# Kernel optimization log

Measured on AMD Instinct MI355X. Metric: run time of the kernel, lower is better.

The kernel has to match this reference:

```python
import jax, jax.numpy as jnp
import numpy as np

N = 50000
E = 800000
IN_C = 128
HID = 64
HEADS = 4
OUT_C = 64
NEG_SLOPE = 0.2


def _glorot(key, shape):
    fan = shape[0] + shape[-1]
    return jax.random.normal(key, shape, dtype=jnp.float32) * jnp.sqrt(2.0 / fan)


def setup_inputs() -> dict:
    key = jax.random.key(0)
    ks = jax.random.split(key, 12)
    x = jax.random.normal(ks[0], (N, IN_C), dtype=jnp.float32)
    edge_index = jax.random.randint(ks[1], (2, E), 0, N, dtype=jnp.int64)
    edge_attr = jax.random.normal(ks[2], (E, 8), dtype=jnp.float32)
    # gat1: in -> heads*hid
    W1 = _glorot(ks[3], (IN_C, HEADS * HID))
    att_src1 = _glorot(ks[4], (HEADS, HID))
    att_dst1 = _glorot(ks[5], (HEADS, HID))
    b1 = jnp.zeros((HEADS * HID,), dtype=jnp.float32)
    # gat2: heads*hid -> out, 1 head
    W2 = _glorot(ks[6], (HEADS * HID, OUT_C))
    att_src2 = _glorot(ks[7], (1, OUT_C))
    att_dst2 = _glorot(ks[8], (1, OUT_C))
    b2 = jnp.zeros((OUT_C,), dtype=jnp.float32)
    return {"x": x, "edge_index": edge_index, "edge_attr": edge_attr,
            "W1": W1, "att_src1": att_src1, "att_dst1": att_dst1, "b1": b1,
            "W2": W2, "att_src2": att_src2, "att_dst2": att_dst2, "b2": b2}


def _gat_conv(x, src, dst, W, att_src, att_dst, b, heads, n_nodes):
    # x: [N, Cin] -> h: [N, H, C]
    h = (x @ W).reshape(n_nodes, heads, -1)
    a_src = jnp.sum(h * att_src, axis=-1)  # [N, H]
    a_dst = jnp.sum(h * att_dst, axis=-1)  # [N, H]
    e = jax.nn.leaky_relu(a_src[src] + a_dst[dst], NEG_SLOPE)  # [Etot, H]
    # segment softmax over destination node (self-loops guarantee non-empty segments)
    m = jax.ops.segment_max(e, dst, num_segments=n_nodes)      # [N, H]
    w = jnp.exp(e - m[dst])
    denom = jax.ops.segment_sum(w, dst, num_segments=n_nodes)  # [N, H]
    alpha = w / (denom[dst] + 1e-16)                           # [Etot, H]
    out = jax.ops.segment_sum(alpha[:, :, None] * h[src], dst, num_segments=n_nodes)
    return out.reshape(n_nodes, -1) + b  # concat heads (identity when heads==1)


def reference(x, edge_index, edge_attr, W1, att_src1, att_dst1, b1, W2, att_src2, att_dst2, b2):
    # PyG GATConv with edge_dim=None ignores edge_attr; add_self_loops=True by default.
    loop = jnp.arange(N, dtype=edge_index.dtype)
    src = jnp.concatenate([edge_index[0], loop])
    dst = jnp.concatenate([edge_index[1], loop])
    h = jax.nn.elu(_gat_conv(x, src, dst, W1, att_src1, att_dst1, b1, HEADS, N))
    out = jax.nn.elu(_gat_conv(h, src, dst, W2, att_src2, att_dst2, b2, 1, N))
    return out
```

## Files before the change

### kernel.cpp

```cpp
#include <hip/hip_runtime.h>
#include <hip/hip_bf16.h>
#include <math.h>

#define LEAKY 0.2f

#define BM 64
#define BN 64
#define BK 32
__global__ __launch_bounds__(256) void gemm_f32(const float* __restrict__ A,
                                                const float* __restrict__ B,
                                                float* __restrict__ C,
                                                int M, int K, int NC) {
    __shared__ float As[BK][BM + 1];
    __shared__ float Bs[BK][BN];
    const int tid = threadIdx.x;
    const int bm = blockIdx.x * BM;
    const int bn = blockIdx.y * BN;
    const int tx = tid & 15, ty = tid >> 4;
    float acc[4][4] = {};
    for (int k0 = 0; k0 < K; k0 += BK) {
        #pragma unroll
        for (int i = 0; i < (BM * BK) / 256; ++i) {
            int idx = tid + i * 256;
            int r = idx >> 5, c = idx & 31;
            int gr = bm + r;
            As[c][r] = (gr < M) ? A[gr * K + k0 + c] : 0.f;
        }
        #pragma unroll
        for (int i = 0; i < (BK * BN) / 256; ++i) {
            int idx = tid + i * 256;
            int r = idx >> 6, c = idx & 63;
            Bs[r][c] = B[(k0 + r) * NC + bn + c];
        }
        __syncthreads();
        #pragma unroll
        for (int k = 0; k < BK; ++k) {
            float a[4], b[4];
            #pragma unroll
            for (int i = 0; i < 4; ++i) a[i] = As[k][ty * 4 + i];
            #pragma unroll
            for (int j = 0; j < 4; ++j) b[j] = Bs[k][tx * 4 + j];
            #pragma unroll
            for (int i = 0; i < 4; ++i)
                #pragma unroll
                for (int j = 0; j < 4; ++j)
                    acc[i][j] += a[i] * b[j];
        }
        __syncthreads();
    }
    #pragma unroll
    for (int i = 0; i < 4; ++i) {
        int gr = bm + ty * 4 + i;
        if (gr < M) {
            #pragma unroll
            for (int j = 0; j < 4; ++j)
                C[gr * NC + bn + tx * 4 + j] = acc[i][j];
        }
    }
}

__global__ __launch_bounds__(256) void attn_scores(const float* __restrict__ h,
                                                   const float* __restrict__ att_s,
                                                   const float* __restrict__ att_d,
                                                   float* __restrict__ asrc,
                                                   float* __restrict__ adst,
                                                   int nN, int HC) {
    int idx = blockIdx.x * 256 + threadIdx.x;
    int lane = threadIdx.x & 63;
    int n = idx / HC;
    int w = idx - n * HC;
    if (n >= nN) return;
    float hv = h[(size_t)n * HC + w];
    float vs = hv * att_s[w];
    float vd = hv * att_d[w];
    #pragma unroll
    for (int off = 32; off > 0; off >>= 1) {
        vs += __shfl_down(vs, off);
        vd += __shfl_down(vd, off);
    }
    if (lane == 0) {
        int head = w >> 6;
        int H = HC >> 6;
        asrc[n * H + head] = vs;
        adst[n * H + head] = vd;
    }
}

__global__ __launch_bounds__(256) void count_deg(const int* __restrict__ ei, int E_, int N_,
                                                 int* __restrict__ deg) {
    int eid = blockIdx.x * 256 + threadIdx.x;
    int Etot = E_ + N_;
    if (eid >= Etot) return;
    int dst = (eid < E_) ? ei[E_ + eid] : (eid - E_);
    atomicAdd(&deg[dst], 1);
}

__global__ __launch_bounds__(1024) void scan_offsets(const int* __restrict__ deg,
                                                     int* __restrict__ off, int n) {
    __shared__ int wsum[16];
    int tid = threadIdx.x;
    int lane = tid & 63, w = tid >> 6;
    int chunk = (n + 1023) / 1024;
    int b = tid * chunk;
    int e = min(b + chunk, n);
    int s = 0;
    for (int i = b; i < e; ++i) s += deg[i];
    int v = s;
    #pragma unroll
    for (int o = 1; o < 64; o <<= 1) {
        int t = __shfl_up(v, o);
        if (lane >= o) v += t;
    }
    if (lane == 63) wsum[w] = v;
    __syncthreads();
    if (w == 0) {
        int t = (lane < 16) ? wsum[lane] : 0;
        #pragma unroll
        for (int o = 1; o < 16; o <<= 1) {
            int u = __shfl_up(t, o);
            if (lane >= o) t += u;
        }
        if (lane < 16) wsum[lane] = t;
    }
    __syncthreads();
    int acc = (w > 0 ? wsum[w - 1] : 0) + (v - s);
    for (int i = b; i < e; ++i) { off[i] = acc; acc += deg[i]; }
    if (e == n) off[n] = acc;
}

__global__ __launch_bounds__(256) void scatter_edges(const int* __restrict__ ei, int E_, int N_,
                                                     int* __restrict__ off,
                                                     int* __restrict__ csr) {
    int eid = blockIdx.x * 256 + threadIdx.x;
    int Etot = E_ + N_;
    if (eid >= Etot) return;
    int src, dst;
    if (eid < E_) { src = ei[eid]; dst = ei[E_ + eid]; }
    else          { src = dst = eid - E_; }
    int pos = atomicAdd(&off[dst], 1);
    csr[pos] = src;
}

__global__ __launch_bounds__(256) void gat_agg_h4(const int* __restrict__ off,
                                                  const int* __restrict__ csr,
                                                  const float* __restrict__ asrc,
                                                  const float* __restrict__ adst,
                                                  const float* __restrict__ hsrc,
                                                  const float* __restrict__ bias,
                                                  float* __restrict__ outp, int N_) {
    int wv = threadIdx.x >> 6, lane = threadIdx.x & 63;
    int node = blockIdx.x * 4 + wv;
    if (node >= N_) return;
    int s = node ? off[node - 1] : 0;
    int e = off[node];
    float4 ad = *(const float4*)(adst + node * 4);
    float m0 = -INFINITY, m1 = -INFINITY, m2 = -INFINITY, m3 = -INFINITY;
    for (int i = s + lane; i < e; i += 64) {
        int u = csr[i];
        float4 as = *(const float4*)(asrc + u * 4);
        float e0 = as.x + ad.x; e0 = e0 > 0.f ? e0 : LEAKY * e0; m0 = fmaxf(m0, e0);
        float e1 = as.y + ad.y; e1 = e1 > 0.f ? e1 : LEAKY * e1; m1 = fmaxf(m1, e1);
        float e2 = as.z + ad.z; e2 = e2 > 0.f ? e2 : LEAKY * e2; m2 = fmaxf(m2, e2);
        float e3 = as.w + ad.w; e3 = e3 > 0.f ? e3 : LEAKY * e3; m3 = fmaxf(m3, e3);
    }
    #pragma unroll
    for (int o = 32; o > 0; o >>= 1) {
        m0 = fmaxf(m0, __shfl_xor(m0, o));
        m1 = fmaxf(m1, __shfl_xor(m1, o));
        m2 = fmaxf(m2, __shfl_xor(m2, o));
        m3 = fmaxf(m3, __shfl_xor(m3, o));
    }
    float a0 = 0.f, a1 = 0.f, a2 = 0.f, a3 = 0.f;
    float d0 = 0.f, d1 = 0.f, d2 = 0.f, d3 = 0.f;
    for (int i = s; i < e; ++i) {
        int u = csr[i];
        float4 as = *(const float4*)(asrc + u * 4);
        float e0 = as.x + ad.x; e0 = e0 > 0.f ? e0 : LEAKY * e0; float w0 = __expf(e0 - m0);
        float e1 = as.y + ad.y; e1 = e1 > 0.f ? e1 : LEAKY * e1; float w1 = __expf(e1 - m1);
        float e2 = as.z + ad.z; e2 = e2 > 0.f ? e2 : LEAKY * e2; float w2 = __expf(e2 - m2);
        float e3 = as.w + ad.w; e3 = e3 > 0.f ? e3 : LEAKY * e3; float w3 = __expf(e3 - m3);
        d0 += w0; d1 += w1; d2 += w2; d3 += w3;
        const float* hp = hsrc + (size_t)u * 256 + lane;
        a0 += w0 * hp[0];
        a1 += w1 * hp[64];
        a2 += w2 * hp[128];
        a3 += w3 * hp[192];
    }
    size_t ob = (size_t)node * 256 + lane;
    float v;
    v = a0 / (d0 + 1e-16f) + bias[lane];       outp[ob]       = v > 0.f ? v : expm1f(v);
    v = a1 / (d1 + 1e-16f) + bias[lane + 64];  outp[ob + 64]  = v > 0.f ? v : expm1f(v);
    v = a2 / (d2 + 1e-16f) + bias[lane + 128]; outp[ob + 128] = v > 0.f ? v : expm1f(v);
    v = a3 / (d3 + 1e-16f) + bias[lane + 192]; outp[ob + 192] = v > 0.f ? v : expm1f(v);
}

__global__ __launch_bounds__(256) void gat_agg_h1(const int* __restrict__ off,
                                                  const int* __restrict__ csr,
                                                  const float* __restrict__ asrc,
                                                  const float* __restrict__ adst,
                                                  const float* __restrict__ g,
                                                  const float* __restrict__ bias,
                                                  float* __restrict__ outp, int N_) {
    int wv = threadIdx.x >> 6, lane = threadIdx.x & 63;
    int node = blockIdx.x * 4 + wv;
    if (node >= N_) return;
    int s = node ? off[node - 1] : 0;
    int e = off[node];
    float ad = adst[node];
    float mm = -INFINITY;
    for (int i = s + lane; i < e; i += 64) {
        float ev = asrc[csr[i]] + ad;
        ev = ev > 0.f ? ev : LEAKY * ev;
        mm = fmaxf(mm, ev);
    }
    #pragma unroll
    for (int o = 32; o > 0; o >>= 1) mm = fmaxf(mm, __shfl_xor(mm, o));
    float a = 0.f, d = 0.f;
    for (int i = s; i < e; ++i) {
        int u = csr[i];
        float ev = asrc[u] + ad;
        ev = ev > 0.f ? ev : LEAKY * ev;
        float w = __expf(ev - mm);
        d += w;
        a += w * g[(size_t)u * 64 + lane];
    }
    float v = a / (d + 1e-16f) + bias[lane];
    outp[(size_t)node * 64 + lane] = v > 0.f ? v : expm1f(v);
}

extern "C" void kernel_launch(void* const* d_in, const int* in_sizes, int n_in,
                              void* d_out, int out_size, void* d_ws, size_t ws_size,
                              hipStream_t stream) {
    const float* x        = (const float*)d_in[0];
    const int*   ei       = (const int*)d_in[1];
    const float* W1       = (const float*)d_in[3];
    const float* att_src1 = (const float*)d_in[4];
    const float* att_dst1 = (const float*)d_in[5];
    const float* b1       = (const float*)d_in[6];
    const float* W2       = (const float*)d_in[7];
    const float* att_src2 = (const float*)d_in[8];
    const float* att_dst2 = (const float*)d_in[9];
    const float* b2       = (const float*)d_in[10];
    float* out = (float*)d_out;

    const int N = in_sizes[0] / 128;
    const int E = in_sizes[1] / 2;
    const int Etot = E + N;

    float* ws    = (float*)d_ws;
    float* h1    = ws;
    float* h2    = h1 + (size_t)N * 256;
    float* g2    = h1;
    float* asrc1 = h2 + (size_t)N * 256;
    float* adst1 = asrc1 + (size_t)N * 4;
    float* asrc2 = adst1 + (size_t)N * 4;
    float* adst2 = asrc2 + N;
    int*   deg   = (int*)(adst2 + N);
    int*   off   = deg + (N + 1);
    int*   csr   = off + (N + 1);

    hipMemsetAsync(deg, 0, (N + 1) * sizeof(int), stream);
    count_deg<<<(Etot + 255) / 256, 256, 0, stream>>>(ei, E, N, deg);
    scan_offsets<<<1, 1024, 0, stream>>>(deg, off, N);
    scatter_edges<<<(Etot + 255) / 256, 256, 0, stream>>>(ei, E, N, off, csr);

    {
        dim3 g((N + BM - 1) / BM, 256 / BN);
        gemm_f32<<<g, 256, 0, stream>>>(x, W1, h1, N, 128, 256);
    }
    attn_scores<<<(N * 256) / 256, 256, 0, stream>>>(h1, att_src1, att_dst1, asrc1, adst1, N, 256);
    gat_agg_h4<<<(N + 3) / 4, 256, 0, stream>>>(off, csr, asrc1, adst1, h1, b1, h2, N);

    {
        dim3 g((N + BM - 1) / BM, 64 / BN);
        gemm_f32<<<g, 256, 0, stream>>>(h2, W2, g2, N, 256, 64);
    }
    attn_scores<<<(N * 64) / 256, 256, 0, stream>>>(g2, att_src2, att_dst2, asrc2, adst2, N, 64);
    gat_agg_h1<<<(N + 3) / 4, 256, 0, stream>>>(off, csr, asrc2, adst2, g2, b2, out, N);
}
```

Before: 628.4 us.

## Fuse attention-score dot products into GEMM epilogue and split h4 aggregation per head

The attention score reductions are computed inside the GEMM epilogue through a 16-lane shuffle reduction, which removes the two separate attn_scores launches and their re-reads of h. The 4-head aggregation kernel now uses one block per node with one wave per head, so each wave handles a single head instead of all four. This spreads the per-node serial edge loop across four waves, but each wave now repeats the CSR index and score loads.

Measured after the change: 705.6 us. +12.3%, slower.

```diff
diff --git a/kernel.cpp b/kernel.cpp
--- a/kernel.cpp
+++ b/kernel.cpp
@@ -7,9 +7,13 @@
 #define BM 64
 #define BN 64
 #define BK 32
-__global__ __launch_bounds__(256) void gemm_f32(const float* __restrict__ A,
+__global__ __launch_bounds__(256) void gemm_att(const float* __restrict__ A,
                                                 const float* __restrict__ B,
                                                 float* __restrict__ C,
+                                                const float* __restrict__ att_s,
+                                                const float* __restrict__ att_d,
+                                                float* __restrict__ asrc,
+                                                float* __restrict__ adst,
                                                 int M, int K, int NC) {
     __shared__ float As[BK][BM + 1];
     __shared__ float Bs[BK][BN];
@@ -24,13 +28,13 @@
             int idx = tid + i * 256;
             int r = idx >> 5, c = idx & 31;
             int gr = bm + r;
-            As[c][r] = (gr < M) ? A[gr * K + k0 + c] : 0.f;
+            As[c][r] = (gr < M) ? A[(size_t)gr * K + k0 + c] : 0.f;
         }
         #pragma unroll
         for (int i = 0; i < (BK * BN) / 256; ++i) {
             int idx = tid + i * 256;
             int r = idx >> 6, c = idx & 63;
-            Bs[r][c] = B[(k0 + r) * NC + bn + c];
+            Bs[r][c] = B[(size_t)(k0 + r) * NC + bn + c];
         }
         __syncthreads();
         #pragma unroll
@@ -48,41 +52,37 @@
         }
         __syncthreads();
     }
+    float s_att[4], d_att[4];
+    #pragma unroll
+    for (int j = 0; j < 4; ++j) {
+        s_att[j] = att_s[bn + tx * 4 + j];
+        d_att[j] = att_d[bn + tx * 4 + j];
+    }
+    const int head = bn >> 6;
+    const int H = NC >> 6;
     #pragma unroll
     for (int i = 0; i < 4; ++i) {
         int gr = bm + ty * 4 + i;
+        float ps = 0.f, pd = 0.f;
+        #pragma unroll
+        for (int j = 0; j < 4; ++j) {
+            ps += acc[i][j] * s_att[j];
+            pd += acc[i][j] * d_att[j];
+        }
+        #pragma unroll
+        for (int o = 1; o < 16; o <<= 1) {
+            ps += __shfl_xor(ps, o);
+            pd += __shfl_xor(pd, o);
+        }
         if (gr < M) {
             #pragma unroll
             for (int j = 0; j < 4; ++j)
-                C[gr * NC + bn + tx * 4 + j] = acc[i][j];
-        }
-    }
-}
-
-__global__ __launch_bounds__(256) void attn_scores(const float* __restrict__ h,
-                                                   const float* __restrict__ att_s,
-                                                   const float* __restrict__ att_d,
-                                                   float* __restrict__ asrc,
-                                                   float* __restrict__ adst,
-                                                   int nN, int HC) {
-    int idx = blockIdx.x * 256 + threadIdx.x;
-    int lane = threadIdx.x & 63;
-    int n = idx / HC;
-    int w = idx - n * HC;
-    if (n >= nN) return;
-    float hv = h[(size_t)n * HC + w];
-    float vs = hv * att_s[w];
-    float vd = hv * att_d[w];
-    #pragma unroll
-    for (int off = 32; off > 0; off >>= 1) {
-        vs += __shfl_down(vs, off);
-        vd += __shfl_down(vd, off);
-    }
-    if (lane == 0) {
-        int head = w >> 6;
-        int H = HC >> 6;
-        asrc[n * H + head] = vs;
-        adst[n * H + head] = vd;
+                C[(size_t)gr * NC + bn + tx * 4 + j] = acc[i][j];
+            if (tx == 0) {
+                asrc[gr * H + head] = ps;
+                adst[gr * H + head] = pd;
+            }
+        }
     }
 }
 
@@ -148,50 +148,32 @@
                                                   const float* __restrict__ hsrc,
                                                   const float* __restrict__ bias,
                                                   float* __restrict__ outp, int N_) {
-    int wv = threadIdx.x >> 6, lane = threadIdx.x & 63;
-    int node = blockIdx.x * 4 + wv;
+    int head = threadIdx.x >> 6;
+    int lane = threadIdx.x & 63;
+    int node = blockIdx.x;
     if (node >= N_) return;
     int s = node ? off[node - 1] : 0;
     int e = off[node];
-    float4 ad = *(const float4*)(adst + node * 4);
-    float m0 = -INFINITY, m1 = -INFINITY, m2 = -INFINITY, m3 = -INFINITY;
+    float ad = adst[node * 4 + head];
+    float m = -INFINITY;
     for (int i = s + lane; i < e; i += 64) {
-        int u = csr[i];
-        float4 as = *(const float4*)(asrc + u * 4);
-        float e0 = as.x + ad.x; e0 = e0 > 0.f ? e0 : LEAKY * e0; m0 = fmaxf(m0, e0);
-        float e1 = as.y + ad.y; e1 = e1 > 0.f ? e1 : LEAKY * e1; m1 = fmaxf(m1, e1);
-        float e2 = as.z + ad.z; e2 = e2 > 0.f ? e2 : LEAKY * e2; m2 = fmaxf(m2, e2);
-        float e3 = as.w + ad.w; e3 = e3 > 0.f ? e3 : LEAKY * e3; m3 = fmaxf(m3, e3);
-    }
-    #pragma unroll
-    for (int o = 32; o > 0; o >>= 1) {
-        m0 = fmaxf(m0, __shfl_xor(m0, o));
-        m1 = fmaxf(m1, __shfl_xor(m1, o));
-        m2 = fmaxf(m2, __shfl_xor(m2, o));
-        m3 = fmaxf(m3, __shfl_xor(m3, o));
-    }
-    float a0 = 0.f, a1 = 0.f, a2 = 0.f, a3 = 0.f;
-    float d0 = 0.f, d1 = 0.f, d2 = 0.f, d3 = 0.f;
+        float ev = asrc[csr[i] * 4 + head] + ad;
+        ev = ev > 0.f ? ev : LEAKY * ev;
+        m = fmaxf(m, ev);
+    }
+    #pragma unroll
+    for (int o = 32; o > 0; o >>= 1) m = fmaxf(m, __shfl_xor(m, o));
+    float a = 0.f, d = 0.f;
     for (int i = s; i < e; ++i) {
         int u = csr[i];
-        float4 as = *(const float4*)(asrc + u * 4);
-        float e0 = as.x + ad.x; e0 = e0 > 0.f ? e0 : LEAKY * e0; float w0 = __expf(e0 - m0);
-        float e1 = as.y + ad.y; e1 = e1 > 0.f ? e1 : LEAKY * e1; float w1 = __expf(e1 - m1);
-        float e2 = as.z + ad.z; e2 = e2 > 0.f ? e2 : LEAKY * e2; float w2 = __expf(e2 - m2);
-        float e3 = as.w + ad.w; e3 = e3 > 0.f ? e3 : LEAKY * e3; float w3 = __expf(e3 - m3);
-        d0 += w0; d1 += w1; d2 += w2; d3 += w3;
-        const float* hp = hsrc + (size_t)u * 256 + lane;
-        a0 += w0 * hp[0];
-        a1 += w1 * hp[64];
-        a2 += w2 * hp[128];
-        a3 += w3 * hp[192];
-    }
-    size_t ob = (size_t)node * 256 + lane;
-    float v;
-    v = a0 / (d0 + 1e-16f) + bias[lane];       outp[ob]       = v > 0.f ? v : expm1f(v);
-    v = a1 / (d1 + 1e-16f) + bias[lane + 64];  outp[ob + 64]  = v > 0.f ? v : expm1f(v);
-    v = a2 / (d2 + 1e-16f) + bias[lane + 128]; outp[ob + 128] = v > 0.f ? v : expm1f(v);
-    v = a3 / (d3 + 1e-16f) + bias[lane + 192]; outp[ob + 192] = v > 0.f ? v : expm1f(v);
+        float ev = asrc[u * 4 + head] + ad;
+        ev = ev > 0.f ? ev : LEAKY * ev;
+        float w = __expf(ev - m);
+        d += w;
+        a += w * hsrc[(size_t)u * 256 + head * 64 + lane];
+    }
+    float v = a / (d + 1e-16f) + bias[head * 64 + lane];
+    outp[(size_t)node * 256 + head * 64 + lane] = v > 0.f ? v : expm1f(v);
 }
 
 __global__ __launch_bounds__(256) void gat_agg_h1(const int* __restrict__ off,
@@ -266,15 +248,13 @@
 
     {
         dim3 g((N + BM - 1) / BM, 256 / BN);
-        gemm_f32<<<g, 256, 0, stream>>>(x, W1, h1, N, 128, 256);
-    }
-    attn_scores<<<(N * 256) / 256, 256, 0, stream>>>(h1, att_src1, att_dst1, asrc1, adst1, N, 256);
-    gat_agg_h4<<<(N + 3) / 4, 256, 0, stream>>>(off, csr, asrc1, adst1, h1, b1, h2, N);
+        gemm_att<<<g, 256, 0, stream>>>(x, W1, h1, att_src1, att_dst1, asrc1, adst1, N, 128, 256);
+    }
+    gat_agg_h4<<<N, 256, 0, stream>>>(off, csr, asrc1, adst1, h1, b1, h2, N);
 
     {
         dim3 g((N + BM - 1) / BM, 64 / BN);
-        gemm_f32<<<g, 256, 0, stream>>>(h2, W2, g2, N, 256, 64);
-    }
-    attn_scores<<<(N * 64) / 256, 256, 0, stream>>>(g2, att_src2, att_dst2, asrc2, adst2, N, 64);
+        gemm_att<<<g, 256, 0, stream>>>(h2, W2, g2, att_src2, att_dst2, asrc2, adst2, N, 256, 64);
+    }
     gat_agg_h1<<<(N + 3) / 4, 256, 0, stream>>>(off, csr, asrc2, adst2, g2, b2, out, N);
 }
```
